# Kernel optimization log

Measured on AMD Instinct MI355X. Metric: run time of the kernel, lower is better.

## Reference

```python
import jax, jax.numpy as jnp
import numpy as np

B, C, H, W = 16, 256, 64, 64
NH, HD, NM = 4, 32, 4  # heads, head_dim, memory tokens
HID = NH * HD


def rms_norm(x, g):
    # F.normalize(x, dim=1) * sqrt(C) * g  (channel dim = 1)
    norm = jnp.maximum(jnp.linalg.norm(x, axis=1, keepdims=True), 1e-12)
    return x / norm * (x.shape[1] ** 0.5) * g


def setup_inputs() -> dict:
    key = jax.random.key(0)
    ks = jax.random.split(key, 5)
    return {
        "x": jax.random.normal(ks[0], (B, C, H, W), jnp.float32),
        "g_in": jnp.ones((1, C, 1, 1), jnp.float32),
        "mem_kv": jax.random.normal(ks[1], (2, NH, HD, NM), jnp.float32),
        "w_qkv": jax.random.normal(ks[2], (HID * 3, C), jnp.float32) * (C ** -0.5),
        "w_out": jax.random.normal(ks[3], (C, HID), jnp.float32) * (HID ** -0.5),
        "b_out": jnp.zeros((C,), jnp.float32),
        "g_out": jnp.ones((1, C, 1, 1), jnp.float32),
    }


def reference(x, g_in, mem_kv, w_qkv, w_out, b_out, g_out):
    b, c, h, w = x.shape
    n = h * w
    scale = HD ** -0.5

    xn = rms_norm(x, g_in)
    # 1x1 conv as matmul over channel dim: [B, 3*HID, H, W]
    qkv = jnp.einsum('oc,bchw->bohw', w_qkv, xn)
    q, k, v = jnp.split(qkv, 3, axis=1)
    # b (h d) x y -> b h d n
    q = q.reshape(b, NH, HD, n)
    k = k.reshape(b, NH, HD, n)
    v = v.reshape(b, NH, HD, n)

    # prepend memory key/value tokens: [b, h, d, NM + n]
    mk = jnp.broadcast_to(mem_kv[0], (b, NH, HD, NM))
    mv = jnp.broadcast_to(mem_kv[1], (b, NH, HD, NM))
    k = jnp.concatenate([mk, k], axis=-1)
    v = jnp.concatenate([mv, v], axis=-1)

    q = jax.nn.softmax(q, axis=-2) * scale  # softmax over head_dim
    k = jax.nn.softmax(k, axis=-1)          # softmax over tokens

    context = jnp.einsum('bhdn,bhen->bhde', k, v)  # [b, h, d, e]
    out = jnp.einsum('bhde,bhdn->bhen', context, q)  # [b, h, e, n]
    out = out.reshape(b, HID, h, w)

    out = jnp.einsum('oc,bchw->bohw', w_out, out) + b_out[None, :, None, None]
    return rms_norm(out, g_out)
```

## Files before the change

### kernel.cpp

```cpp
#include <hip/hip_runtime.h>
#include <math.h>

typedef unsigned short u16;
typedef unsigned int u32;

#define NBATCH 16
#define NCH    256
#define NPIX   4096
#define NHEAD  4
#define HDIM   32
#define NMEM   4
#define HID    128
#define OC3    384
#define SCALE_Q 0.17677669529663687f

typedef __bf16 bf16x8 __attribute__((ext_vector_type(8)));
typedef float  f32x4  __attribute__((ext_vector_type(4)));

__device__ __forceinline__ u16 bfb(float f){
  union { __bf16 h; u16 u; } x; x.h = (__bf16)f; return x.u;
}
__device__ __forceinline__ u32 pkbf2(float a, float b){
  union { __bf16 h[2]; u32 u; } x; x.h[0] = (__bf16)a; x.h[1] = (__bf16)b; return x.u;
}
__device__ __forceinline__ void gload_lds16(const void* gp, void* lp){
  __builtin_amdgcn_global_load_lds(
      (const __attribute__((address_space(1))) unsigned int*)gp,
      (__attribute__((address_space(3))) unsigned int*)lp, 16, 0, 0);
}

__global__ __launch_bounds__(256) void k_pack(const float* __restrict__ wqkv,
                                              const float* __restrict__ gin,
                                              const float* __restrict__ wout,
                                              u16* __restrict__ wqb,
                                              u16* __restrict__ wob)
{
  int i = blockIdx.x*256 + threadIdx.x;
  if (i < OC3*NCH){ int c = i & 255; wqb[i] = bfb(wqkv[i]*gin[c]); }
  else { int j = i - OC3*NCH; wob[j] = bfb(wout[j]); }
}

__global__ __launch_bounds__(512, 4) void k_qkvx(const float* __restrict__ x,
                                                 const u16* __restrict__ wqb,
                                                 u16* __restrict__ qt,
                                                 float* __restrict__ ctxp2)
{
  __shared__ __align__(16) char smem[52480];
  float (*Xs)[64]   = (float(*)[64])smem;
  u16*   Bx         = (u16*)(smem + 16384);
  float (*ssqp)[64] = (float(*)[64])(smem + 50176);
  float* rl         = (float*)(smem + 52224);
  u16*   Ek         = (u16*)smem;
  u16*   Vv         = (u16*)(smem + 18432);
  float (*psx)[64]  = (float(*)[64])(smem + 36864);

  const int t = threadIdx.x, w = t>>6, lane = t&63;
  const int n0 = blockIdx.x*64, b = blockIdx.y;
  const int qw = lane>>4, rr = lane&15;

  {
    float ssq = 0.f;
    for (int s=0;s<4;++s){
      asm volatile("s_waitcnt lgkmcnt(0)" ::: "memory");
      const float* gp = x + ((size_t)b*NCH + s*64 + w*8 + (lane>>4))*NPIX + n0 + (lane&15)*4;
      gload_lds16(gp,                    &Xs[w*8 + 0][0]);
      gload_lds16(gp + (size_t)4*NPIX,   &Xs[w*8 + 4][0]);
      asm volatile("s_waitcnt vmcnt(0)" ::: "memory");
      u32 pk[4];
      #pragma unroll
      for (int q=0;q<4;q++){
        float v0 = Xs[w*8 + 2*q    ][lane];
        float v1 = Xs[w*8 + 2*q + 1][lane];
        ssq += v0*v0 + v1*v1;
        pk[q] = pkbf2(v0, v1);
      }
      *(int4*)&Bx[lane*264 + s*64 + w*8] = make_int4((int)pk[0],(int)pk[1],(int)pk[2],(int)pk[3]);
    }
    ssqp[w][lane] = ssq;
  }
  __syncthreads();
  if (t < 64){
    float s = 0.f;
    #pragma unroll
    for (int g=0;g<8;g++) s += ssqp[g][t];
    rl[t] = 16.0f / fmaxf(sqrtf(s), 1e-12f);
  }

  f32x4 acc[3][4];
  #pragma unroll
  for (int p=0;p<3;p++)
    #pragma unroll
    for (int nf=0;nf<4;nf++) acc[p][nf] = (f32x4){0.f,0.f,0.f,0.f};

  const u16* aw = wqb + (size_t)(w*16 + rr)*NCH + qw*8;
  bf16x8 caf0 = *(const bf16x8*)(aw);
  bf16x8 caf1 = *(const bf16x8*)(aw + 128*NCH);
  bf16x8 caf2 = *(const bf16x8*)(aw + 256*NCH);
  #pragma unroll
  for (int c0=0; c0<NCH; c0+=32){
    bf16x8 bfr[4];
    #pragma unroll
    for (int nf=0;nf<4;nf++)
      bfr[nf] = *(const bf16x8*)&Bx[(nf*16+rr)*264 + c0 + qw*8];
    bf16x8 naf0 = caf0, naf1 = caf1, naf2 = caf2;
    if (c0 < NCH-32){
      naf0 = *(const bf16x8*)(aw + c0+32);
      naf1 = *(const bf16x8*)(aw + 128*NCH + c0+32);
      naf2 = *(const bf16x8*)(aw + 256*NCH + c0+32);
    }
    #pragma unroll
    for (int nf=0;nf<4;nf++){
      acc[0][nf] = __builtin_amdgcn_mfma_f32_16x16x32_bf16(caf0, bfr[nf], acc[0][nf], 0, 0, 0);
      acc[1][nf] = __builtin_amdgcn_mfma_f32_16x16x32_bf16(bfr[nf], caf1, acc[1][nf], 0, 0, 0);
      acc[2][nf] = __builtin_amdgcn_mfma_f32_16x16x32_bf16(bfr[nf], caf2, acc[2][nf], 0, 0, 0);
    }
    caf0 = naf0; caf1 = naf1; caf2 = naf2;
  }

  __syncthreads();

  float zk = 0.f;
  #pragma unroll
  for (int nf=0;nf<4;nf++){
    const float4 rv4 = *(const float4*)&rl[nf*16 + qw*4];
    float e0 = __expf(acc[1][nf][0]*rv4.x);
    float e1 = __expf(acc[1][nf][1]*rv4.y);
    float e2 = __expf(acc[1][nf][2]*rv4.z);
    float e3 = __expf(acc[1][nf][3]*rv4.w);
    zk += e0+e1+e2+e3;
    *(int2*)&Ek[(w*16+rr)*72 + nf*16 + qw*4] =
        make_int2((int)pkbf2(e0,e1), (int)pkbf2(e2,e3));
    float v0 = acc[2][nf][0]*rv4.x, v1 = acc[2][nf][1]*rv4.y;
    float v2 = acc[2][nf][2]*rv4.z, v3 = acc[2][nf][3]*rv4.w;
    *(int2*)&Vv[(w*16+rr)*72 + nf*16 + qw*4] =
        make_int2((int)pkbf2(v0,v1), (int)pkbf2(v2,v3));
  }
  zk += __shfl_xor(zk, 16, 64);
  zk += __shfl_xor(zk, 32, 64);

  float qv[4][4], pm[4], ps[4];
  #pragma unroll
  for (int nf=0;nf<4;nf++){
    float rv = rl[nf*16 + rr];
    float m = -1e30f;
    #pragma unroll
    for (int r=0;r<4;r++){ qv[nf][r] = acc[0][nf][r]*rv; m = fmaxf(m, qv[nf][r]); }
    m = fmaxf(m, __shfl_xor(m, 16, 64));
    m = fmaxf(m, __shfl_xor(m, 32, 64));
    float s = 0.f;
    #pragma unroll
    for (int r=0;r<4;r++){ qv[nf][r] = __expf(qv[nf][r]-m); s += qv[nf][r]; }
    s += __shfl_xor(s, 16, 64);
    s += __shfl_xor(s, 32, 64);
    pm[nf] = m; ps[nf] = s;
  }
  if (lane < 16){
    #pragma unroll
    for (int nf=0;nf<4;nf++){ ssqp[w][nf*16+lane] = pm[nf]; psx[w][nf*16+lane] = ps[nf]; }
  }
  __syncthreads();
  {
    const int pw = w^1;
    u16* qbase = qt + ((size_t)b*NPIX + n0)*HID + w*16 + qw*4;
    #pragma unroll
    for (int nf=0;nf<4;nf++){
      float om = ssqp[pw][nf*16+rr], os = psx[pw][nf*16+rr];
      float M = fmaxf(pm[nf], om);
      float S = ps[nf]*__expf(pm[nf]-M) + os*__expf(om-M);
      float f = __expf(pm[nf]-M) * SCALE_Q / S;
      u32 lo = pkbf2(qv[nf][0]*f, qv[nf][1]*f);
      u32 hi = pkbf2(qv[nf][2]*f, qv[nf][3]*f);
      *(int2*)(qbase + (size_t)(nf*16+rr)*HID) = make_int2((int)lo,(int)hi);
    }
  }

  {
    const int h = w>>1, eh = w&1;
    f32x4 pacc[2] = {(f32x4){0.f,0.f,0.f,0.f},(f32x4){0.f,0.f,0.f,0.f}};
    #pragma unroll
    for (int ks=0; ks<2; ks++){
      bf16x8 bv = *(const bf16x8*)&Vv[(h*32+eh*16+rr)*72 + ks*32 + qw*8];
      #pragma unroll
      for (int i=0;i<2;i++){
        bf16x8 ae = *(const bf16x8*)&Ek[(h*32+i*16+rr)*72 + ks*32 + qw*8];
        pacc[i] = __builtin_amdgcn_mfma_f32_16x16x32_bf16(ae, bv, pacc[i], 0, 0, 0);
      }
    }
    float* pb = ctxp2 + ((size_t)((b*64 + blockIdx.x)*4 + h))*1088;
    #pragma unroll
    for (int i=0;i<2;i++)
      #pragma unroll
      for (int reg=0;reg<4;reg++)
        pb[(i*16+qw*4+reg)*32 + eh*16 + rr] = pacc[i][reg];
    if (qw==0) pb[1024 + (w&1)*16 + rr] = zk;
  }
}

__global__ __launch_bounds__(256) void k_fin(const float* __restrict__ ctxp2,
                                             const float* __restrict__ memkv,
                                             float* __restrict__ ctx)
{
  const int bh = blockIdx.x, b = bh>>2, h = bh&3, t = threadIdx.x;
  const int d = t>>3, e0 = (t&7)*4;
  float4 ps = make_float4(0.f,0.f,0.f,0.f);
  float z = 0.f;
  for (int s=0;s<64;s++){
    const float* pb = ctxp2 + ((size_t)((b*64+s)*4+h))*1088;
    float4 v = *(const float4*)(pb + d*32 + e0);
    ps.x+=v.x; ps.y+=v.y; ps.z+=v.z; ps.w+=v.w;
    z += pb[1024 + d];
  }
  #pragma unroll
  for (int m=0;m<4;m++){
    float em = __expf(memkv[(h*HDIM+d)*NMEM + m]);
    z += em;
    ps.x += em*memkv[512 + (h*HDIM+e0+0)*NMEM + m];
    ps.y += em*memkv[512 + (h*HDIM+e0+1)*NMEM + m];
    ps.z += em*memkv[512 + (h*HDIM+e0+2)*NMEM + m];
    ps.w += em*memkv[512 + (h*HDIM+e0+3)*NMEM + m];
  }
  float inv = 1.0f/z;
  *(float4*)(ctx + (size_t)bh*1024 + d*32 + e0) =
      make_float4(ps.x*inv, ps.y*inv, ps.z*inv, ps.w*inv);
}

__global__ __launch_bounds__(256) void k_fout(const u16* __restrict__ qt,
                                              const float* __restrict__ ctx,
                                              const u16* __restrict__ wob,
                                              const float* __restrict__ bout,
                                              const float* __restrict__ gout,
                                              float* __restrict__ out)
{
  __shared__ u16 Cb[4*32*40];
  __shared__ u16 Ao[64*136];
  __shared__ float ssql[4][64];
  const int t = threadIdx.x, w = t>>6, lane = t&63;
  const int n0 = blockIdx.x*64, b = blockIdx.y;
  const int qw = lane>>4, rr = lane&15;

  {
    const float4* c4 = (const float4*)(ctx + (size_t)b*4096);
    const int d = (t>>3)&31, e0 = (t&7)*4;
    #pragma unroll
    for (int h=0;h<4;h++){
      float4 v = c4[t + h*256];
      Cb[(h*32+e0+0)*40 + d] = bfb(v.x);
      Cb[(h*32+e0+1)*40 + d] = bfb(v.y);
      Cb[(h*32+e0+2)*40 + d] = bfb(v.z);
      Cb[(h*32+e0+3)*40 + d] = bfb(v.w);
    }
  }
  __syncthreads();

  f32x4 pv[4][2];
  const u16* qp = qt + ((size_t)b*NPIX + n0 + w*16 + rr)*HID;
  #pragma unroll
  for (int h=0;h<4;h++){
    bf16x8 bq = *(const bf16x8*)(qp + h*32 + qw*8);
    #pragma unroll
    for (int ef=0;ef<2;ef++){
      bf16x8 af = *(const bf16x8*)&Cb[(h*32 + ef*16 + rr)*40 + qw*8];
      f32x4 z = (f32x4){0.f,0.f,0.f,0.f};
      pv[h][ef] = __builtin_amdgcn_mfma_f32_16x16x32_bf16(af, bq, z, 0, 0, 0);
    }
  }
  #pragma unroll
  for (int h=0;h<4;h++)
    #pragma unroll
    for (int ef=0;ef<2;ef++){
      u32 lohi0 = pkbf2(pv[h][ef][0], pv[h][ef][1]);
      u32 lohi1 = pkbf2(pv[h][ef][2], pv[h][ef][3]);
      *(int2*)&Ao[(w*16+rr)*136 + h*32 + ef*16 + qw*4] = make_int2((int)lohi0,(int)lohi1);
    }
  __syncthreads();

  f32x4 acc[4][4];
  #pragma unroll
  for (int i=0;i<4;i++)
    #pragma unroll
    for (int j=0;j<4;j++) acc[i][j] = (f32x4){0.f,0.f,0.f,0.f};
  #pragma unroll
  for (int k0=0; k0<HID; k0+=32){
    bf16x8 af[4], bfr[4];
    #pragma unroll
    for (int mf=0;mf<4;mf++)
      af[mf] = *(const bf16x8*)&wob[(size_t)(w*64 + mf*16 + rr)*HID + k0 + qw*8];
    #pragma unroll
    for (int nf=0;nf<4;nf++)
      bfr[nf] = *(const bf16x8*)&Ao[(nf*16+rr)*136 + k0 + qw*8];
    #pragma unroll
    for (int mf=0;mf<4;mf++)
      #pragma unroll
      for (int nf=0;nf<4;nf++)
        acc[mf][nf] = __builtin_amdgcn_mfma_f32_16x16x32_bf16(af[mf], bfr[nf], acc[mf][nf], 0, 0, 0);
  }
  float pssq[4] = {0.f,0.f,0.f,0.f};
  #pragma unroll
  for (int mf=0;mf<4;mf++)
    #pragma unroll
    for (int reg=0;reg<4;reg++){
      int c = w*64 + mf*16 + qw*4 + reg;
      float bb = bout[c];
      #pragma unroll
      for (int nf=0;nf<4;nf++){
        float v = acc[mf][nf][reg] + bb;
        acc[mf][nf][reg] = v;
        pssq[nf] += v*v;
      }
    }
  #pragma unroll
  for (int nf=0;nf<4;nf++){
    pssq[nf] += __shfl_xor(pssq[nf], 16, 64);
    pssq[nf] += __shfl_xor(pssq[nf], 32, 64);
  }
  if (qw==0){
    #pragma unroll
    for (int nf=0;nf<4;nf++) ssql[w][nf*16+rr] = pssq[nf];
  }
  __syncthreads();
  float rv[4];
  #pragma unroll
  for (int nf=0;nf<4;nf++){
    int col = nf*16 + rr;
    float sm = ssql[0][col]+ssql[1][col]+ssql[2][col]+ssql[3][col];
    rv[nf] = 16.0f / fmaxf(sqrtf(sm), 1e-12f);
  }
  #pragma unroll
  for (int mf=0;mf<4;mf++)
    #pragma unroll
    for (int reg=0;reg<4;reg++){
      int c = w*64 + mf*16 + qw*4 + reg;
      float g = gout[c];
      float* po = out + ((size_t)(b*NCH + c))*NPIX + n0;
      #pragma unroll
      for (int nf=0;nf<4;nf++)
        po[nf*16 + rr] = acc[mf][nf][reg]*rv[nf]*g;
    }
}

extern "C" void kernel_launch(void* const* d_in, const int* in_sizes, int n_in,
                              void* d_out, int out_size, void* d_ws, size_t ws_size,
                              hipStream_t stream)
{
  const float* x     = (const float*)d_in[0];
  const float* gin   = (const float*)d_in[1];
  const float* memkv = (const float*)d_in[2];
  const float* wqkv  = (const float*)d_in[3];
  const float* wout  = (const float*)d_in[4];
  const float* bout  = (const float*)d_in[5];
  const float* gout  = (const float*)d_in[6];
  float* out = (float*)d_out;

  char* ws = (char*)d_ws;
  u16*    qt    = (u16*)   (ws);
  float*  ctxp2 = (float*) (ws + 16777216);
  float*  ctx   = (float*) (ws + 34603008);
  u16*    wqb   = (u16*)   (ws + 34865152);
  u16*    wob   = (u16*)   (ws + 35061760);
  hipLaunchKernelGGL(k_pack, dim3(512),   dim3(256), 0, stream, wqkv, gin, wout, wqb, wob);
  hipLaunchKernelGGL(k_qkvx, dim3(64,16), dim3(512), 0, stream, x, wqb, qt, ctxp2);
  hipLaunchKernelGGL(k_fin,  dim3(64),    dim3(256), 0, stream, ctxp2, memkv, ctx);
  hipLaunchKernelGGL(k_fout, dim3(64,16), dim3(256), 0, stream, qt, ctx, wob, bout, gout, out);
}
```

Measured before the change: 172.5 us.

## Replace per-tile context partials and reduce kernel with global atomics

The per-tile context and normalizer partials that k_fin used to sum are now accumulated directly into a per-batch buffer with atomicAdd from k_qkvx. The memory-token contributions are precomputed in k_pack, and the final normalization is folded into k_fout's LDS staging. This removes one kernel launch and the 17MB partial-buffer write and read, at the cost of a memset, heavy atomic contention on 4K floats per batch from 64 blocks, and nondeterministic summation order.

```diff
diff --git a/kernel.cpp b/kernel.cpp
--- a/kernel.cpp
+++ b/kernel.cpp
@@ -32,18 +32,39 @@
 __global__ __launch_bounds__(256) void k_pack(const float* __restrict__ wqkv,
                                               const float* __restrict__ gin,
                                               const float* __restrict__ wout,
+                                              const float* __restrict__ memkv,
                                               u16* __restrict__ wqb,
-                                              u16* __restrict__ wob)
+                                              u16* __restrict__ wob,
+                                              float* __restrict__ ctxmem,
+                                              float* __restrict__ zmem)
 {
   int i = blockIdx.x*256 + threadIdx.x;
   if (i < OC3*NCH){ int c = i & 255; wqb[i] = bfb(wqkv[i]*gin[c]); }
-  else { int j = i - OC3*NCH; wob[j] = bfb(wout[j]); }
+  else if (i < OC3*NCH + NCH*HID){ int j = i - OC3*NCH; wob[j] = bfb(wout[j]); }
+  else {
+    int j = i - (OC3*NCH + NCH*HID);
+    if (j < 4096){
+      int h = j>>10, d = (j>>5)&31, e = j&31;
+      float s = 0.f;
+      #pragma unroll
+      for (int m=0;m<4;m++)
+        s += __expf(memkv[(h*HDIM+d)*NMEM + m]) * memkv[512 + (h*HDIM+e)*NMEM + m];
+      ctxmem[j] = s;
+    } else if (j < 4224){
+      int k = j - 4096; int h = k>>5, d = k&31;
+      float s = 0.f;
+      #pragma unroll
+      for (int m=0;m<4;m++) s += __expf(memkv[(h*HDIM+d)*NMEM + m]);
+      zmem[k] = s;
+    }
+  }
 }
 
 __global__ __launch_bounds__(512, 4) void k_qkvx(const float* __restrict__ x,
                                                  const u16* __restrict__ wqb,
                                                  u16* __restrict__ qt,
-                                                 float* __restrict__ ctxp2)
+                                                 float* __restrict__ ctxa,
+                                                 float* __restrict__ za)
 {
   __shared__ __align__(16) char smem[52480];
   float (*Xs)[64]   = (float(*)[64])smem;
@@ -186,46 +207,21 @@
         pacc[i] = __builtin_amdgcn_mfma_f32_16x16x32_bf16(ae, bv, pacc[i], 0, 0, 0);
       }
     }
-    float* pb = ctxp2 + ((size_t)((b*64 + blockIdx.x)*4 + h))*1088;
+    float* pb = ctxa + (size_t)b*4096 + h*1024;
     #pragma unroll
     for (int i=0;i<2;i++)
       #pragma unroll
       for (int reg=0;reg<4;reg++)
-        pb[(i*16+qw*4+reg)*32 + eh*16 + rr] = pacc[i][reg];
-    if (qw==0) pb[1024 + (w&1)*16 + rr] = zk;
-  }
-}
-
-__global__ __launch_bounds__(256) void k_fin(const float* __restrict__ ctxp2,
-                                             const float* __restrict__ memkv,
-                                             float* __restrict__ ctx)
-{
-  const int bh = blockIdx.x, b = bh>>2, h = bh&3, t = threadIdx.x;
-  const int d = t>>3, e0 = (t&7)*4;
-  float4 ps = make_float4(0.f,0.f,0.f,0.f);
-  float z = 0.f;
-  for (int s=0;s<64;s++){
-    const float* pb = ctxp2 + ((size_t)((b*64+s)*4+h))*1088;
-    float4 v = *(const float4*)(pb + d*32 + e0);
-    ps.x+=v.x; ps.y+=v.y; ps.z+=v.z; ps.w+=v.w;
-    z += pb[1024 + d];
-  }
-  #pragma unroll
-  for (int m=0;m<4;m++){
-    float em = __expf(memkv[(h*HDIM+d)*NMEM + m]);
-    z += em;
-    ps.x += em*memkv[512 + (h*HDIM+e0+0)*NMEM + m];
-    ps.y += em*memkv[512 + (h*HDIM+e0+1)*NMEM + m];
-    ps.z += em*memkv[512 + (h*HDIM+e0+2)*NMEM + m];
-    ps.w += em*memkv[512 + (h*HDIM+e0+3)*NMEM + m];
-  }
-  float inv = 1.0f/z;
-  *(float4*)(ctx + (size_t)bh*1024 + d*32 + e0) =
-      make_float4(ps.x*inv, ps.y*inv, ps.z*inv, ps.w*inv);
+        atomicAdd(&pb[(i*16+qw*4+reg)*32 + eh*16 + rr], pacc[i][reg]);
+    if (qw==0) atomicAdd(&za[b*128 + w*16 + rr], zk);
+  }
 }
 
 __global__ __launch_bounds__(256) void k_fout(const u16* __restrict__ qt,
-                                              const float* __restrict__ ctx,
+                                              const float* __restrict__ ctxa,
+                                              const float* __restrict__ za,
+                                              const float* __restrict__ ctxmem,
+                                              const float* __restrict__ zmem,
                                               const u16* __restrict__ wob,
                                               const float* __restrict__ bout,
                                               const float* __restrict__ gout,
@@ -239,15 +235,16 @@
   const int qw = lane>>4, rr = lane&15;
 
   {
-    const float4* c4 = (const float4*)(ctx + (size_t)b*4096);
     const int d = (t>>3)&31, e0 = (t&7)*4;
     #pragma unroll
     for (int h=0;h<4;h++){
-      float4 v = c4[t + h*256];
-      Cb[(h*32+e0+0)*40 + d] = bfb(v.x);
-      Cb[(h*32+e0+1)*40 + d] = bfb(v.y);
-      Cb[(h*32+e0+2)*40 + d] = bfb(v.z);
-      Cb[(h*32+e0+3)*40 + d] = bfb(v.w);
+      float4 a = *(const float4*)(ctxa + (size_t)b*4096 + h*1024 + d*32 + e0);
+      float4 m = *(const float4*)(ctxmem + h*1024 + d*32 + e0);
+      float rinv = 1.0f / (za[b*128 + h*32 + d] + zmem[h*32 + d]);
+      Cb[(h*32+e0+0)*40 + d] = bfb((a.x+m.x)*rinv);
+      Cb[(h*32+e0+1)*40 + d] = bfb((a.y+m.y)*rinv);
+      Cb[(h*32+e0+2)*40 + d] = bfb((a.z+m.z)*rinv);
+      Cb[(h*32+e0+3)*40 + d] = bfb((a.w+m.w)*rinv);
     }
   }
   __syncthreads();
@@ -352,13 +349,19 @@
   float* out = (float*)d_out;
 
   char* ws = (char*)d_ws;
-  u16*    qt    = (u16*)   (ws);
-  float*  ctxp2 = (float*) (ws + 16777216);
-  float*  ctx   = (float*) (ws + 34603008);
-  u16*    wqb   = (u16*)   (ws + 34865152);
-  u16*    wob   = (u16*)   (ws + 35061760);
-  hipLaunchKernelGGL(k_pack, dim3(512),   dim3(256), 0, stream, wqkv, gin, wout, wqb, wob);
-  hipLaunchKernelGGL(k_qkvx, dim3(64,16), dim3(512), 0, stream, x, wqb, qt, ctxp2);
-  hipLaunchKernelGGL(k_fin,  dim3(64),    dim3(256), 0, stream, ctxp2, memkv, ctx);
-  hipLaunchKernelGGL(k_fout, dim3(64,16), dim3(256), 0, stream, qt, ctx, wob, bout, gout, out);
-}
+  u16*    qt     = (u16*)   (ws);
+  float*  ctxa   = (float*) (ws + 16777216);
+  float*  za     = (float*) (ws + 17039360);
+  float*  ctxmem = (float*) (ws + 17047552);
+  float*  zmem   = (float*) (ws + 17063936);
+  u16*    wqb    = (u16*)   (ws + 17064448);
+  u16*    wob    = (u16*)   (ws + 17261056);
+
+  hipMemsetAsync(ws + 16777216, 0, 270336, stream);
+
+  hipLaunchKernelGGL(k_pack, dim3(529),   dim3(256), 0, stream,
+                     wqkv, gin, wout, memkv, wqb, wob, ctxmem, zmem);
+  hipLaunchKernelGGL(k_qkvx, dim3(64,16), dim3(512), 0, stream, x, wqb, qt, ctxa, za);
+  hipLaunchKernelGGL(k_fout, dim3(64,16), dim3(256), 0, stream,
+                     qt, ctxa, za, ctxmem, zmem, wob, bout, gout, out);
+}
```

Measured after the change: 175.4 us. About the same (+1.7%).
